# Kernel optimization log

Measured on AMD Instinct MI355X. Metric: run time of the kernel, lower is better.

The kernel has to match this reference:

```python
import jax, jax.numpy as jnp
import numpy as np

C = 128
DW = 2 * C   # dw_expansion_rate = 2
FF = 2 * C   # ffn_expansion_rate = 2
EPS = 1e-6   # flax LayerNorm default


def _layernorm(x, scale, bias):
    mu = jnp.mean(x, axis=-1, keepdims=True)
    var = jnp.mean(jnp.square(x - mu), axis=-1, keepdims=True)
    return (x - mu) * jax.lax.rsqrt(var + EPS) * scale + bias


def setup_inputs() -> dict:
    key = jax.random.key(0)
    ks = jax.random.split(key, 20)
    s = 0.05
    return {
        "x": jax.random.normal(ks[0], (8, 192, 192, C), jnp.float32),
        "ln1_scale": jnp.ones((C,), jnp.float32),
        "ln1_bias": jnp.zeros((C,), jnp.float32),
        "w1": jax.random.normal(ks[1], (C, DW), jnp.float32) * s,   # 1x1 conv expand
        "b1": jax.random.normal(ks[2], (DW,), jnp.float32) * s,
        "wdw": jax.random.normal(ks[3], (DW,), jnp.float32) * s,    # 1x1 depthwise == per-channel scale
        "bdw": jax.random.normal(ks[4], (DW,), jnp.float32) * s,
        "wse": jax.random.normal(ks[5], (C, C), jnp.float32) * s,   # SE dense
        "bse": jax.random.normal(ks[6], (C,), jnp.float32) * s,
        "w2": jax.random.normal(ks[7], (C, C), jnp.float32) * s,    # 1x1 conv project
        "b2": jax.random.normal(ks[8], (C,), jnp.float32) * s,
        "ln2_scale": jnp.ones((C,), jnp.float32),
        "ln2_bias": jnp.zeros((C,), jnp.float32),
        "wf1": jax.random.normal(ks[9], (C, FF), jnp.float32) * s,  # FFN expand
        "bf1": jax.random.normal(ks[10], (FF,), jnp.float32) * s,
        "wf2": jax.random.normal(ks[11], (C, C), jnp.float32) * s,  # FFN project
        "bf2": jax.random.normal(ks[12], (C,), jnp.float32) * s,
        "beta": jax.random.normal(ks[13], (1, 1, 1, C), jnp.float32) * s,
        "gamma": jax.random.normal(ks[14], (1, 1, 1, C), jnp.float32) * s,
    }


def reference(x, ln1_scale, ln1_bias, w1, b1, wdw, bdw, wse, bse, w2, b2,
              ln2_scale, ln2_bias, wf1, bf1, wf2, bf2, beta, gamma):
    # --- spatial branch ---
    s = _layernorm(x, ln1_scale, ln1_bias)
    s = jnp.einsum('bhwc,cd->bhwd', s, w1) + b1            # 1x1 conv, C -> 2C
    s = s * wdw + bdw                                      # 1x1 depthwise conv (per-channel affine)
    g1, g2 = jnp.split(s, 2, axis=-1)
    s = g1 * g2                                            # SimpleGate, back to C channels
    gap = jnp.mean(s, axis=(1, 2), keepdims=True)          # [B,1,1,C]
    att = jnp.einsum('bijc,cd->bijd', gap, wse) + bse      # SE dense
    s = s * att
    s = jnp.einsum('bhwc,cd->bhwd', s, w2) + b2            # 1x1 conv project
    x = x + beta * s
    # --- channel (FFN) branch ---
    c = _layernorm(x, ln2_scale, ln2_bias)
    c = jnp.einsum('bhwc,cd->bhwd', c, wf1) + bf1          # Dense, C -> 2C
    c1, c2 = jnp.split(c, 2, axis=-1)
    c = c1 * c2                                            # SimpleGate
    c = jnp.einsum('bhwc,cd->bhwd', c, wf2) + bf2          # Dense project
    return x + gamma * c
```

## Files before the change

kernel.cpp:

```cpp
#include <hip/hip_runtime.h>
#include <cstddef>

#define C_    128
#define DW_   256
#define HW_   (192 * 192)
#define B_    8
#define NPIX_ (B_ * HW_)
#define EPS_  1e-6f
#define PA_   136

typedef __bf16 bf16_t;
typedef __bf16 bf16x8 __attribute__((ext_vector_type(8)));
typedef __bf16 bf16x4 __attribute__((ext_vector_type(4)));
typedef float  f32x4  __attribute__((ext_vector_type(4)));

__device__ __forceinline__ float4 ld4(const float* p) { return *(const float4*)p; }

__global__ void k_prep(const float* __restrict__ w1, const float* __restrict__ b1,
                       const float* __restrict__ wdw, const float* __restrict__ bdw,
                       const float* __restrict__ w2, const float* __restrict__ wf1,
                       const float* __restrict__ wf2,
                       bf16_t* __restrict__ wt1, bf16_t* __restrict__ wt2,
                       bf16_t* __restrict__ wtf1, bf16_t* __restrict__ wtf2,
                       float* __restrict__ b1f, float* __restrict__ gap)
{
    const int id = blockIdx.x * blockDim.x + threadIdx.x;
    const int stride = gridDim.x * blockDim.x;
    for (int n = id; n < B_ * C_; n += stride)
        gap[n] = 0.f;
    for (int n = id; n < DW_; n += stride)
        b1f[n] = b1[n] * wdw[n] + bdw[n];
    for (int f = id; f < 32768; f += stride) {
        const int j = f & 7, lane = (f >> 3) & 63, s = (f >> 9) & 3, t = f >> 11;
        const int n = t * 16 + (lane & 15);
        const int k = s * 32 + ((lane >> 4) << 3) + j;
        wt1[f] = (bf16_t)(w1[k * DW_ + n] * wdw[n]);
    }
    for (int f = id; f < 16384; f += stride) {
        const int j = f & 7, lane = (f >> 3) & 63, s = (f >> 9) & 3, t = f >> 11;
        const int n = t * 16 + (lane & 15);
        const int k = s * 32 + ((lane >> 4) << 3) + j;
        wt2[f] = (bf16_t)(w2[k * C_ + n]);
    }
    for (int f = id; f < 32768; f += stride) {
        const int j = f & 7, lane = (f >> 3) & 63, s = (f >> 9) & 3, t = f >> 11;
        const int n = t * 16 + (lane & 15);
        const int k = s * 32 + ((lane >> 4) << 3) + j;
        wtf1[f] = (bf16_t)(wf1[k * DW_ + n]);
    }
    for (int f = id; f < 16384; f += stride) {
        const int j = f & 7, lane = (f >> 3) & 63, s = (f >> 9) & 3, t = f >> 11;
        const int n = t * 16 + (lane & 15);
        const int k = s * 32 + ((lane >> 4) << 3) + j;
        wtf2[f] = (bf16_t)(wf2[k * C_ + n]);
    }
}

template<int SGBF>
__global__ __launch_bounds__(256) void k_phase1(
    const float* __restrict__ x,
    const float* __restrict__ ln1s, const float* __restrict__ ln1b,
    const bf16_t* __restrict__ wt1, const float* __restrict__ b1f,
    float* __restrict__ sg_f, bf16_t* __restrict__ sg_h,
    float* __restrict__ gap)
{
    __shared__ __align__(16) bf16_t sA[64 * PA_];
    __shared__ float sRed[4 * C_];
    const int tid = threadIdx.x;
    const int pix0 = blockIdx.x * 64;
    const int batch = pix0 / HW_;

    {
        const int p = tid >> 2, sub = tid & 3;
        const float* xr = x + (size_t)(pix0 + p) * C_ + sub * 32;
        float4 v[8];
        float s = 0.f, ss = 0.f;
        #pragma unroll
        for (int u = 0; u < 8; u++) {
            v[u] = ld4(xr + u * 4);
            s  += v[u].x + v[u].y + v[u].z + v[u].w;
            ss += v[u].x * v[u].x + v[u].y * v[u].y + v[u].z * v[u].z + v[u].w * v[u].w;
        }
        s += __shfl_xor(s, 1); ss += __shfl_xor(ss, 1);
        s += __shfl_xor(s, 2); ss += __shfl_xor(ss, 2);
        const float mu  = s * (1.f / C_);
        const float var = ss * (1.f / C_) - mu * mu;
        const float rr  = rsqrtf(var + EPS_);
        #pragma unroll
        for (int u = 0; u < 8; u++) {
            const int c0 = sub * 32 + u * 4;
            const float4 sc = ld4(ln1s + c0), bi = ld4(ln1b + c0);
            bf16x4 o;
            o[0] = (bf16_t)((v[u].x - mu) * rr * sc.x + bi.x);
            o[1] = (bf16_t)((v[u].y - mu) * rr * sc.y + bi.y);
            o[2] = (bf16_t)((v[u].z - mu) * rr * sc.z + bi.z);
            o[3] = (bf16_t)((v[u].w - mu) * rr * sc.w + bi.w);
            *(bf16x4*)(&sA[p * PA_ + c0]) = o;
        }
    }
    __syncthreads();

    const int lane = tid & 63, wave = tid >> 6;
    const int l15 = lane & 15, quad = lane >> 4;

    bf16x8 af[4];
    #pragma unroll
    for (int s = 0; s < 4; s++)
        af[s] = *(const bf16x8*)(&sA[(wave * 16 + l15) * PA_ + s * 32 + quad * 8]);

    float gacc[8];
    #pragma unroll
    for (int t = 0; t < 8; t++) {
        f32x4 a0 = {0.f, 0.f, 0.f, 0.f};
        f32x4 a1 = {0.f, 0.f, 0.f, 0.f};
        #pragma unroll
        for (int s = 0; s < 4; s++) {
            const bf16x8 b0 = *(const bf16x8*)(wt1 + ((size_t)((t    ) * 4 + s) * 64 + lane) * 8);
            const bf16x8 b1 = *(const bf16x8*)(wt1 + ((size_t)((t + 8) * 4 + s) * 64 + lane) * 8);
            a0 = __builtin_amdgcn_mfma_f32_16x16x32_bf16(af[s], b0, a0, 0, 0, 0);
            a1 = __builtin_amdgcn_mfma_f32_16x16x32_bf16(af[s], b1, a1, 0, 0, 0);
        }
        const float bb0 = b1f[t * 16 + l15], bb1 = b1f[128 + t * 16 + l15];
        float gs = 0.f;
        #pragma unroll
        for (int r = 0; r < 4; r++) {
            const float g = (a0[r] + bb0) * (a1[r] + bb1);
            const size_t idx = (size_t)(pix0 + wave * 16 + quad * 4 + r) * C_ + t * 16 + l15;
            if constexpr (SGBF) sg_h[idx] = (bf16_t)g;
            else                sg_f[idx] = g;
            gs += g;
        }
        gacc[t] = gs;
    }

    #pragma unroll
    for (int t = 0; t < 8; t++) {
        float g = gacc[t];
        g += __shfl_xor(g, 16);
        g += __shfl_xor(g, 32);
        if (lane < 16) sRed[wave * C_ + t * 16 + lane] = g;
    }
    __syncthreads();
    if (tid < C_) {
        const float s4 = sRed[tid] + sRed[C_ + tid] + sRed[2 * C_ + tid] + sRed[3 * C_ + tid];
        atomicAdd(&gap[batch * C_ + tid], s4);
    }
}

__global__ __launch_bounds__(128) void k_se(
    const float* __restrict__ gap, const float* __restrict__ wse,
    const float* __restrict__ bse, float* __restrict__ att)
{
    const int b = blockIdx.x;
    const int d = threadIdx.x;
    float acc = bse[d];
    const float inv = 1.0f / (float)HW_;
    for (int cc = 0; cc < C_; cc++)
        acc = fmaf(gap[b * C_ + cc] * inv, wse[cc * C_ + d], acc);
    att[b * C_ + d] = acc;
}

template<int SGBF>
__global__ __launch_bounds__(256) void k_phase2(
    const float* __restrict__ x, const float* __restrict__ att,
    const bf16_t* __restrict__ wt2, const float* __restrict__ b2,
    const float* __restrict__ ln2s, const float* __restrict__ ln2b,
    const bf16_t* __restrict__ wtf1, const float* __restrict__ bf1,
    const bf16_t* __restrict__ wtf2, const float* __restrict__ bf2,
    const float* __restrict__ beta, const float* __restrict__ gamma,
    const float* __restrict__ sg_f, const bf16_t* __restrict__ sg_h,
    float* __restrict__ out)
{
    __shared__ __align__(16) bf16_t sA[64 * PA_];
    __shared__ __align__(16) float  ybuf[64 * 132];
    bf16_t* cgb = (bf16_t*)ybuf;

    const int tid = threadIdx.x;
    const int pix0 = blockIdx.x * 64;
    const int batch = pix0 / HW_;

    {
        const int p = tid >> 2, sub = tid & 3;
        const float* ar = att + batch * C_ + sub * 32;
        if constexpr (SGBF) {
            const bf16_t* gr = sg_h + (size_t)(pix0 + p) * C_ + sub * 32;
            #pragma unroll
            for (int u = 0; u < 4; u++) {
                const bf16x8 g = *(const bf16x8*)(gr + u * 8);
                const float4 a0 = ld4(ar + u * 8), a1 = ld4(ar + u * 8 + 4);
                bf16x8 o;
                o[0] = (bf16_t)((float)g[0] * a0.x);
                o[1] = (bf16_t)((float)g[1] * a0.y);
                o[2] = (bf16_t)((float)g[2] * a0.z);
                o[3] = (bf16_t)((float)g[3] * a0.w);
                o[4] = (bf16_t)((float)g[4] * a1.x);
                o[5] = (bf16_t)((float)g[5] * a1.y);
                o[6] = (bf16_t)((float)g[6] * a1.z);
                o[7] = (bf16_t)((float)g[7] * a1.w);
                *(bf16x8*)(&sA[p * PA_ + sub * 32 + u * 8]) = o;
            }
        } else {
            const float* gr = sg_f + (size_t)(pix0 + p) * C_ + sub * 32;
            #pragma unroll
            for (int u = 0; u < 8; u++) {
                const float4 g = ld4(gr + u * 4), a = ld4(ar + u * 4);
                bf16x4 o;
                o[0] = (bf16_t)(g.x * a.x);
                o[1] = (bf16_t)(g.y * a.y);
                o[2] = (bf16_t)(g.z * a.z);
                o[3] = (bf16_t)(g.w * a.w);
                *(bf16x4*)(&sA[p * PA_ + sub * 32 + u * 4]) = o;
            }
        }
    }
    __syncthreads();

    const int lane = tid & 63, wave = tid >> 6;
    const int l15 = lane & 15, quad = lane >> 4;
    float yreg[32];

    {
        bf16x8 af[4];
        #pragma unroll
        for (int s = 0; s < 4; s++)
            af[s] = *(const bf16x8*)(&sA[(wave * 16 + l15) * PA_ + s * 32 + quad * 8]);
        #pragma unroll
        for (int t = 0; t < 8; t++) {
            f32x4 acc = {0.f, 0.f, 0.f, 0.f};
            #pragma unroll
            for (int s = 0; s < 4; s++) {
                const bf16x8 b = *(const bf16x8*)(wt2 + ((size_t)(t * 4 + s) * 64 + lane) * 8);
                acc = __builtin_amdgcn_mfma_f32_16x16x32_bf16(af[s], b, acc, 0, 0, 0);
            }
            const int n = t * 16 + l15;
            const float b2n = b2[n], bta = beta[n];
            #pragma unroll
            for (int r = 0; r < 4; r++) {
                const int m = wave * 16 + quad * 4 + r;
                const float xv = x[(size_t)(pix0 + m) * C_ + n];
                const float yv = xv + bta * (acc[r] + b2n);
                yreg[t * 4 + r] = yv;
                ybuf[m * 132 + n] = yv;
            }
        }
    }
    __syncthreads();

    {
        const int p = tid >> 2, sub = tid & 3;
        float4 v[8];
        float s = 0.f, ss = 0.f;
        #pragma unroll
        for (int u = 0; u < 8; u++) {
            v[u] = *(const float4*)(&ybuf[p * 132 + sub * 32 + u * 4]);
            s  += v[u].x + v[u].y + v[u].z + v[u].w;
            ss += v[u].x * v[u].x + v[u].y * v[u].y + v[u].z * v[u].z + v[u].w * v[u].w;
        }
        s += __shfl_xor(s, 1); ss += __shfl_xor(ss, 1);
        s += __shfl_xor(s, 2); ss += __shfl_xor(ss, 2);
        const float mu  = s * (1.f / C_);
        const float var = ss * (1.f / C_) - mu * mu;
        const float rr  = rsqrtf(var + EPS_);
        #pragma unroll
        for (int u = 0; u < 8; u++) {
            const int c0 = sub * 32 + u * 4;
            const float4 sc = ld4(ln2s + c0), bi = ld4(ln2b + c0);
            bf16x4 o;
            o[0] = (bf16_t)((v[u].x - mu) * rr * sc.x + bi.x);
            o[1] = (bf16_t)((v[u].y - mu) * rr * sc.y + bi.y);
            o[2] = (bf16_t)((v[u].z - mu) * rr * sc.z + bi.z);
            o[3] = (bf16_t)((v[u].w - mu) * rr * sc.w + bi.w);
            *(bf16x4*)(&sA[p * PA_ + c0]) = o;
        }
    }
    __syncthreads();

    {
        bf16x8 af[4];
        #pragma unroll
        for (int s = 0; s < 4; s++)
            af[s] = *(const bf16x8*)(&sA[(wave * 16 + l15) * PA_ + s * 32 + quad * 8]);
        #pragma unroll
        for (int t = 0; t < 8; t++) {
            f32x4 a0 = {0.f, 0.f, 0.f, 0.f};
            f32x4 a1 = {0.f, 0.f, 0.f, 0.f};
            #pragma unroll
            for (int s = 0; s < 4; s++) {
                const bf16x8 b0 = *(const bf16x8*)(wtf1 + ((size_t)((t    ) * 4 + s) * 64 + lane) * 8);
                const bf16x8 b1 = *(const bf16x8*)(wtf1 + ((size_t)((t + 8) * 4 + s) * 64 + lane) * 8);
                a0 = __builtin_amdgcn_mfma_f32_16x16x32_bf16(af[s], b0, a0, 0, 0, 0);
                a1 = __builtin_amdgcn_mfma_f32_16x16x32_bf16(af[s], b1, a1, 0, 0, 0);
            }
            const float f1a = bf1[t * 16 + l15], f1b = bf1[128 + t * 16 + l15];
            #pragma unroll
            for (int r = 0; r < 4; r++) {
                const float cg = (a0[r] + f1a) * (a1[r] + f1b);
                cgb[(wave * 16 + quad * 4 + r) * PA_ + t * 16 + l15] = (bf16_t)cg;
            }
        }
    }
    __syncthreads();

    {
        bf16x8 af[4];
        #pragma unroll
        for (int s = 0; s < 4; s++)
            af[s] = *(const bf16x8*)(&cgb[(wave * 16 + l15) * PA_ + s * 32 + quad * 8]);
        #pragma unroll
        for (int t = 0; t < 8; t++) {
            f32x4 acc = {0.f, 0.f, 0.f, 0.f};
            #pragma unroll
            for (int s = 0; s < 4; s++) {
                const bf16x8 b = *(const bf16x8*)(wtf2 + ((size_t)(t * 4 + s) * 64 + lane) * 8);
                acc = __builtin_amdgcn_mfma_f32_16x16x32_bf16(af[s], b, acc, 0, 0, 0);
            }
            const int n = t * 16 + l15;
            const float fb = bf2[n], gm = gamma[n];
            #pragma unroll
            for (int r = 0; r < 4; r++) {
                const int m = wave * 16 + quad * 4 + r;
                out[(size_t)(pix0 + m) * C_ + n] = yreg[t * 4 + r] + gm * (acc[r] + fb);
            }
        }
    }
}

extern "C" void kernel_launch(void* const* d_in, const int* in_sizes, int n_in,
                              void* d_out, int out_size, void* d_ws, size_t ws_size,
                              hipStream_t stream)
{
    const float* x     = (const float*)d_in[0];
    const float* ln1s  = (const float*)d_in[1];
    const float* ln1b  = (const float*)d_in[2];
    const float* w1    = (const float*)d_in[3];
    const float* b1    = (const float*)d_in[4];
    const float* wdw   = (const float*)d_in[5];
    const float* bdw   = (const float*)d_in[6];
    const float* wse   = (const float*)d_in[7];
    const float* bse   = (const float*)d_in[8];
    const float* w2    = (const float*)d_in[9];
    const float* b2    = (const float*)d_in[10];
    const float* ln2s  = (const float*)d_in[11];
    const float* ln2b  = (const float*)d_in[12];
    const float* wf1   = (const float*)d_in[13];
    const float* bf1   = (const float*)d_in[14];
    const float* wf2   = (const float*)d_in[15];
    const float* bf2   = (const float*)d_in[16];
    const float* beta  = (const float*)d_in[17];
    const float* gamma = (const float*)d_in[18];

    float* out = (float*)d_out;
    char*  ws  = (char*)d_ws;
    float*  gap  = (float*)(ws);
    float*  attb = (float*)(ws + 4096);
    float*  b1f  = (float*)(ws + 8192);
    bf16_t* wt1  = (bf16_t*)(ws + 12288);
    bf16_t* wt2  = (bf16_t*)(ws + 77824);
    bf16_t* wtf1 = (bf16_t*)(ws + 110592);
    bf16_t* wtf2 = (bf16_t*)(ws + 176128);

    const size_t SG_OFF   = (size_t)1 << 20;
    const size_t SG_BYTES = (size_t)NPIX_ * C_ * sizeof(bf16_t);
    const bool   use_bf   = (ws_size >= SG_OFF + SG_BYTES);
    bf16_t* sgh = (bf16_t*)(ws + SG_OFF);

    k_prep<<<192, 256, 0, stream>>>(w1, b1, wdw, bdw, w2, wf1, wf2,
                                    wt1, wt2, wtf1, wtf2, b1f, gap);
    if (use_bf) {
        k_phase1<1><<<NPIX_ / 64, 256, 0, stream>>>(x, ln1s, ln1b, wt1, b1f,
                                                    out, sgh, gap);
        k_se<<<B_, C_, 0, stream>>>(gap, wse, bse, attb);
        k_phase2<1><<<NPIX_ / 64, 256, 0, stream>>>(x, attb, wt2, b2, ln2s, ln2b,
                                                    wtf1, bf1, wtf2, bf2, beta, gamma,
                                                    out, sgh, out);
    } else {
        k_phase1<0><<<NPIX_ / 64, 256, 0, stream>>>(x, ln1s, ln1b, wt1, b1f,
                                                    out, sgh, gap);
        k_se<<<B_, C_, 0, stream>>>(gap, wse, bse, attb);
        k_phase2<0><<<NPIX_ / 64, 256, 0, stream>>>(x, attb, wt2, b2, ln2s, ln2b,
                                                    wtf1, bf1, wtf2, bf2, beta, gamma,
                                                    out, sgh, out);
    }
}
```

Measured before the change: 511.0 us.

## Split MFMA work across waves by output columns to cut weight fetches

Each wave now owns two 16-column output tiles across all 64 pixels, instead of 16 pixels across all columns, in every GEMM stage. It loads its B-weight fragments once into registers and reuses them for four M tiles, cutting global and L2 weight traffic per block by about four times. The cost is four times more LDS reads of A fragments. Because each GAP channel now belongs to a single wave, the cross-wave shared-memory reduction in phase 1 is simpler. Phase 2 also issues the residual x loads at kernel start so they overlap with the LayerNorm and SE-scaling work.

```diff
diff --git a/kernel.cpp b/kernel.cpp
--- a/kernel.cpp
+++ b/kernel.cpp
@@ -65,7 +65,7 @@
     float* __restrict__ gap)
 {
     __shared__ __align__(16) bf16_t sA[64 * PA_];
-    __shared__ float sRed[4 * C_];
+    __shared__ float sRed[C_];
     const int tid = threadIdx.x;
     const int pix0 = blockIdx.x * 64;
     const int batch = pix0 / HW_;
@@ -103,48 +103,46 @@
     const int lane = tid & 63, wave = tid >> 6;
     const int l15 = lane & 15, quad = lane >> 4;
 
-    bf16x8 af[4];
     #pragma unroll
-    for (int s = 0; s < 4; s++)
-        af[s] = *(const bf16x8*)(&sA[(wave * 16 + l15) * PA_ + s * 32 + quad * 8]);
-
-    float gacc[8];
-    #pragma unroll
-    for (int t = 0; t < 8; t++) {
-        f32x4 a0 = {0.f, 0.f, 0.f, 0.f};
-        f32x4 a1 = {0.f, 0.f, 0.f, 0.f};
+    for (int tt = 0; tt < 2; tt++) {
+        const int t = wave * 2 + tt;
+        bf16x8 b0[4], b1[4];
         #pragma unroll
         for (int s = 0; s < 4; s++) {
-            const bf16x8 b0 = *(const bf16x8*)(wt1 + ((size_t)((t    ) * 4 + s) * 64 + lane) * 8);
-            const bf16x8 b1 = *(const bf16x8*)(wt1 + ((size_t)((t + 8) * 4 + s) * 64 + lane) * 8);
-            a0 = __builtin_amdgcn_mfma_f32_16x16x32_bf16(af[s], b0, a0, 0, 0, 0);
-            a1 = __builtin_amdgcn_mfma_f32_16x16x32_bf16(af[s], b1, a1, 0, 0, 0);
+            b0[s] = *(const bf16x8*)(wt1 + ((size_t)((t    ) * 4 + s) * 64 + lane) * 8);
+            b1[s] = *(const bf16x8*)(wt1 + ((size_t)((t + 8) * 4 + s) * 64 + lane) * 8);
         }
         const float bb0 = b1f[t * 16 + l15], bb1 = b1f[128 + t * 16 + l15];
         float gs = 0.f;
         #pragma unroll
-        for (int r = 0; r < 4; r++) {
-            const float g = (a0[r] + bb0) * (a1[r] + bb1);
-            const size_t idx = (size_t)(pix0 + wave * 16 + quad * 4 + r) * C_ + t * 16 + l15;
-            if constexpr (SGBF) sg_h[idx] = (bf16_t)g;
-            else                sg_f[idx] = g;
-            gs += g;
-        }
-        gacc[t] = gs;
-    }
-
-    #pragma unroll
-    for (int t = 0; t < 8; t++) {
-        float g = gacc[t];
-        g += __shfl_xor(g, 16);
-        g += __shfl_xor(g, 32);
-        if (lane < 16) sRed[wave * C_ + t * 16 + lane] = g;
-    }
-    __syncthreads();
-    if (tid < C_) {
-        const float s4 = sRed[tid] + sRed[C_ + tid] + sRed[2 * C_ + tid] + sRed[3 * C_ + tid];
-        atomicAdd(&gap[batch * C_ + tid], s4);
-    }
+        for (int m = 0; m < 4; m++) {
+            bf16x8 af[4];
+            #pragma unroll
+            for (int s = 0; s < 4; s++)
+                af[s] = *(const bf16x8*)(&sA[(m * 16 + l15) * PA_ + s * 32 + quad * 8]);
+            f32x4 a0 = {0.f, 0.f, 0.f, 0.f};
+            f32x4 a1 = {0.f, 0.f, 0.f, 0.f};
+            #pragma unroll
+            for (int s = 0; s < 4; s++) {
+                a0 = __builtin_amdgcn_mfma_f32_16x16x32_bf16(af[s], b0[s], a0, 0, 0, 0);
+                a1 = __builtin_amdgcn_mfma_f32_16x16x32_bf16(af[s], b1[s], a1, 0, 0, 0);
+            }
+            #pragma unroll
+            for (int r = 0; r < 4; r++) {
+                const float g = (a0[r] + bb0) * (a1[r] + bb1);
+                const size_t idx = (size_t)(pix0 + m * 16 + quad * 4 + r) * C_ + t * 16 + l15;
+                if constexpr (SGBF) sg_h[idx] = (bf16_t)g;
+                else                sg_f[idx] = g;
+                gs += g;
+            }
+        }
+        gs += __shfl_xor(gs, 16);
+        gs += __shfl_xor(gs, 32);
+        if (lane < 16) sRed[t * 16 + lane] = gs;
+    }
+    __syncthreads();
+    if (tid < C_)
+        atomicAdd(&gap[batch * C_ + tid], sRed[tid]);
 }
 
 __global__ __launch_bounds__(128) void k_se(
@@ -178,6 +176,18 @@
     const int tid = threadIdx.x;
     const int pix0 = blockIdx.x * 64;
     const int batch = pix0 / HW_;
+    const int lane = tid & 63, wave = tid >> 6;
+    const int l15 = lane & 15, quad = lane >> 4;
+
+    float xr[2][4][4];
+    #pragma unroll
+    for (int tt = 0; tt < 2; tt++)
+        #pragma unroll
+        for (int m = 0; m < 4; m++)
+            #pragma unroll
+            for (int r = 0; r < 4; r++)
+                xr[tt][m][r] = x[(size_t)(pix0 + m * 16 + quad * 4 + r) * C_
+                                 + (wave * 2 + tt) * 16 + l15];
 
     {
         const int p = tid >> 2, sub = tid & 3;
@@ -215,32 +225,32 @@
     }
     __syncthreads();
 
-    const int lane = tid & 63, wave = tid >> 6;
-    const int l15 = lane & 15, quad = lane >> 4;
-    float yreg[32];
-
-    {
-        bf16x8 af[4];
+    float yreg[2][4][4];
+
+    #pragma unroll
+    for (int tt = 0; tt < 2; tt++) {
+        const int t = wave * 2 + tt;
+        bf16x8 bw[4];
         #pragma unroll
         for (int s = 0; s < 4; s++)
-            af[s] = *(const bf16x8*)(&sA[(wave * 16 + l15) * PA_ + s * 32 + quad * 8]);
-        #pragma unroll
-        for (int t = 0; t < 8; t++) {
+            bw[s] = *(const bf16x8*)(wt2 + ((size_t)(t * 4 + s) * 64 + lane) * 8);
+        const int n = t * 16 + l15;
+        const float b2n = b2[n], bta = beta[n];
+        #pragma unroll
+        for (int m = 0; m < 4; m++) {
+            bf16x8 af[4];
+            #pragma unroll
+            for (int s = 0; s < 4; s++)
+                af[s] = *(const bf16x8*)(&sA[(m * 16 + l15) * PA_ + s * 32 + quad * 8]);
             f32x4 acc = {0.f, 0.f, 0.f, 0.f};
             #pragma unroll
-            for (int s = 0; s < 4; s++) {
-                const bf16x8 b = *(const bf16x8*)(wt2 + ((size_t)(t * 4 + s) * 64 + lane) * 8);
-                acc = __builtin_amdgcn_mfma_f32_16x16x32_bf16(af[s], b, acc, 0, 0, 0);
-            }
-            const int n = t * 16 + l15;
-            const float b2n = b2[n], bta = beta[n];
+            for (int s = 0; s < 4; s++)
+                acc = __builtin_amdgcn_mfma_f32_16x16x32_bf16(af[s], bw[s], acc, 0, 0, 0);
             #pragma unroll
             for (int r = 0; r < 4; r++) {
-                const int m = wave * 16 + quad * 4 + r;
-                const float xv = x[(size_t)(pix0 + m) * C_ + n];
-                const float yv = xv + bta * (acc[r] + b2n);
-                yreg[t * 4 + r] = yv;
-                ybuf[m * 132 + n] = yv;
+                const float yv = xr[tt][m][r] + bta * (acc[r] + b2n);
+                yreg[tt][m][r] = yv;
+                ybuf[(m * 16 + quad * 4 + r) * 132 + n] = yv;
             }
         }
     }
@@ -275,52 +285,61 @@
     }
     __syncthreads();
 
-    {
-        bf16x8 af[4];
-        #pragma unroll
-        for (int s = 0; s < 4; s++)
-            af[s] = *(const bf16x8*)(&sA[(wave * 16 + l15) * PA_ + s * 32 + quad * 8]);
-        #pragma unroll
-        for (int t = 0; t < 8; t++) {
+    #pragma unroll
+    for (int tt = 0; tt < 2; tt++) {
+        const int t = wave * 2 + tt;
+        bf16x8 c0[4], c1[4];
+        #pragma unroll
+        for (int s = 0; s < 4; s++) {
+            c0[s] = *(const bf16x8*)(wtf1 + ((size_t)((t    ) * 4 + s) * 64 + lane) * 8);
+            c1[s] = *(const bf16x8*)(wtf1 + ((size_t)((t + 8) * 4 + s) * 64 + lane) * 8);
+        }
+        const float f1a = bf1[t * 16 + l15], f1b = bf1[128 + t * 16 + l15];
+        #pragma unroll
+        for (int m = 0; m < 4; m++) {
+            bf16x8 af[4];
+            #pragma unroll
+            for (int s = 0; s < 4; s++)
+                af[s] = *(const bf16x8*)(&sA[(m * 16 + l15) * PA_ + s * 32 + quad * 8]);
             f32x4 a0 = {0.f, 0.f, 0.f, 0.f};
             f32x4 a1 = {0.f, 0.f, 0.f, 0.f};
             #pragma unroll
             for (int s = 0; s < 4; s++) {
-                const bf16x8 b0 = *(const bf16x8*)(wtf1 + ((size_t)((t    ) * 4 + s) * 64 + lane) * 8);
-                const bf16x8 b1 = *(const bf16x8*)(wtf1 + ((size_t)((t + 8) * 4 + s) * 64 + lane) * 8);
-                a0 = __builtin_amdgcn_mfma_f32_16x16x32_bf16(af[s], b0, a0, 0, 0, 0);
-                a1 = __builtin_amdgcn_mfma_f32_16x16x32_bf16(af[s], b1, a1, 0, 0, 0);
-            }
-            const float f1a = bf1[t * 16 + l15], f1b = bf1[128 + t * 16 + l15];
+                a0 = __builtin_amdgcn_mfma_f32_16x16x32_bf16(af[s], c0[s], a0, 0, 0, 0);
+                a1 = __builtin_amdgcn_mfma_f32_16x16x32_bf16(af[s], c1[s], a1, 0, 0, 0);
+            }
             #pragma unroll
             for (int r = 0; r < 4; r++) {
                 const float cg = (a0[r] + f1a) * (a1[r] + f1b);
-                cgb[(wave * 16 + quad * 4 + r) * PA_ + t * 16 + l15] = (bf16_t)cg;
-            }
-        }
-    }
-    __syncthreads();
-
-    {
-        bf16x8 af[4];
+                cgb[(m * 16 + quad * 4 + r) * PA_ + t * 16 + l15] = (bf16_t)cg;
+            }
+        }
+    }
+    __syncthreads();
+
+    #pragma unroll
+    for (int tt = 0; tt < 2; tt++) {
+        const int t = wave * 2 + tt;
+        bf16x8 bw[4];
         #pragma unroll
         for (int s = 0; s < 4; s++)
-            af[s] = *(const bf16x8*)(&cgb[(wave * 16 + l15) * PA_ + s * 32 + quad * 8]);
-        #pragma unroll
-        for (int t = 0; t < 8; t++) {
+            bw[s] = *(const bf16x8*)(wtf2 + ((size_t)(t * 4 + s) * 64 + lane) * 8);
+        const int n = t * 16 + l15;
+        const float fb = bf2[n], gm = gamma[n];
+        #pragma unroll
+        for (int m = 0; m < 4; m++) {
+            bf16x8 af[4];
+            #pragma unroll
+            for (int s = 0; s < 4; s++)
+                af[s] = *(const bf16x8*)(&cgb[(m * 16 + l15) * PA_ + s * 32 + quad * 8]);
             f32x4 acc = {0.f, 0.f, 0.f, 0.f};
             #pragma unroll
-            for (int s = 0; s < 4; s++) {
-                const bf16x8 b = *(const bf16x8*)(wtf2 + ((size_t)(t * 4 + s) * 64 + lane) * 8);
-                acc = __builtin_amdgcn_mfma_f32_16x16x32_bf16(af[s], b, acc, 0, 0, 0);
-            }
-            const int n = t * 16 + l15;
-            const float fb = bf2[n], gm = gamma[n];
-            #pragma unroll
-            for (int r = 0; r < 4; r++) {
-                const int m = wave * 16 + quad * 4 + r;
-                out[(size_t)(pix0 + m) * C_ + n] = yreg[t * 4 + r] + gm * (acc[r] + fb);
-            }
+            for (int s = 0; s < 4; s++)
+                acc = __builtin_amdgcn_mfma_f32_16x16x32_bf16(af[s], bw[s], acc, 0, 0, 0);
+            #pragma unroll
+            for (int r = 0; r < 4; r++)
+                out[(size_t)(pix0 + m * 16 + quad * 4 + r) * C_ + n] =
+                    yreg[tt][m][r] + gm * (acc[r] + fb);
         }
     }
 }
```

After: 451.5 us. 11.7% less time.
